# Kernel optimization log

Measured on AMD Instinct MI355X. Metric: run time of the kernel, lower is better.

## Reference

```python
import jax, jax.numpy as jnp
import numpy as np

SOS = 1
H = 1024   # hidden_size
V = 32000  # vocab_size
B = 64     # batch
S = 50     # encoder (source) length
T = 25     # decode steps (target length)


def setup_inputs() -> dict:
    key = jax.random.key(0)
    ks = jax.random.split(key, 16)
    s = 1.0 / np.sqrt(H)

    def u(k, shape):
        return jax.random.uniform(k, shape, jnp.float32, -s, s)

    return {
        "encoder_outputs": jax.random.normal(ks[0], (B, S, H), jnp.float32),
        "encoder_hidden": jax.random.normal(ks[1], (1, B, H), jnp.float32),
        "target_tensor": jax.random.randint(ks[2], (B, T), 0, V),
        "emb": jax.random.normal(ks[3], (V, H), jnp.float32),       # nn.Embedding
        "Wa": u(ks[4], (H, H)), "ba": u(ks[5], (H,)),               # attention query proj
        "Ua": u(ks[6], (H, H)), "bu": u(ks[7], (H,)),               # attention key proj
        "Va": u(ks[8], (H, 1)), "bv": u(ks[9], (1,)),               # attention score vector
        "W_ih": u(ks[10], (3 * H, 2 * H)), "b_ih": u(ks[11], (3 * H,)),  # GRU input weights
        "W_hh": u(ks[12], (3 * H, H)), "b_hh": u(ks[13], (3 * H,)),     # GRU hidden weights
        "Wout": u(ks[14], (V, H)), "bout": u(ks[15], (V,)),         # output linear
    }


def reference(encoder_outputs, encoder_hidden, target_tensor, emb,
              Wa, ba, Ua, bu, Va, bv, W_ih, b_ih, W_hh, b_hh, Wout, bout):
    # Bahdanau key projection is independent of the decode step: precompute once.
    keys_proj = encoder_outputs @ Ua.T + bu        # [B, S, H]
    h0 = encoder_hidden[0]                         # [B, H]

    # Teacher forcing: input at step i is SOS then target[:, :-1]. (Dropout in eval mode = identity.)
    sos = jnp.full((B, 1), SOS, dtype=target_tensor.dtype)
    tokens = jnp.concatenate([sos, target_tensor[:, :-1]], axis=1).T  # [T, B]

    def step(h, tok):
        x_emb = emb[tok]                                         # [B, H]
        q = h @ Wa.T + ba                                        # [B, H] (query = hidden)
        scores = jnp.tanh(q[:, None, :] + keys_proj) @ Va        # [B, S, 1]
        w = jax.nn.softmax(scores[..., 0] + bv[0], axis=-1)      # [B, S]
        context = jnp.einsum('bs,bsh->bh', w, encoder_outputs)   # [B, H]
        x = jnp.concatenate([x_emb, context], axis=-1)           # [B, 2H]
        gx = x @ W_ih.T + b_ih                                   # [B, 3H]
        gh = h @ W_hh.T + b_hh                                   # [B, 3H]
        rx, zx, nx = jnp.split(gx, 3, axis=-1)                   # PyTorch gate order r,z,n
        rh, zh, nh = jnp.split(gh, 3, axis=-1)
        r = jax.nn.sigmoid(rx + rh)
        z = jax.nn.sigmoid(zx + zh)
        n = jnp.tanh(nx + r * nh)
        h_new = (1.0 - z) * n + z * h
        logits = h_new @ Wout.T + bout                           # [B, V]
        return h_new, logits

    _, logits = jax.lax.scan(step, h0, tokens)                   # [T, B, V]
    return jnp.transpose(logits, (1, 0, 2))                      # [B, T, V]
```

## Files before the change

kernel.cpp:

```cpp
#include <hip/hip_runtime.h>
#include <hip/hip_bf16.h>

#define BB_ 64
#define SS_ 50
#define TT_ 25
#define HH_ 1024
#define VV_ 32000

typedef __bf16 bf16x8 __attribute__((ext_vector_type(8)));
typedef float f32x4 __attribute__((ext_vector_type(4)));
typedef unsigned long long u64;

__device__ __forceinline__ unsigned short f2b(float f) {
  unsigned u = __float_as_uint(f);
  u = (u + 0x7FFFu + ((u >> 16) & 1u)) >> 16;
  return (unsigned short)u;
}
__device__ __forceinline__ float b2f_(unsigned short s) {
  return __uint_as_float((unsigned)s << 16);
}
__device__ __forceinline__ float fast_tanh(float x) {
  float e = __expf(2.f * x);
  return 1.f - 2.f / (e + 1.f);
}
__device__ __forceinline__ float fast_sigmoid(float x) {
  return 1.f / (1.f + __expf(-x));
}
__device__ __forceinline__ void gload16(const void* g, void* l) {
  __builtin_amdgcn_global_load_lds((const __attribute__((address_space(1))) void*)g,
                                   (__attribute__((address_space(3))) void*)l, 16, 0, 0);
}
__device__ __forceinline__ bf16x8 ldb8(const unsigned short* p) {
  return *(const bf16x8*)p;
}

__device__ __forceinline__ void cstf(float* p, float v) {
  __hip_atomic_store(p, v, __ATOMIC_RELAXED, __HIP_MEMORY_SCOPE_AGENT);
}
__device__ __forceinline__ void cst4(unsigned* p, unsigned v) {
  __hip_atomic_store(p, v, __ATOMIC_RELAXED, __HIP_MEMORY_SCOPE_AGENT);
}
__device__ __forceinline__ unsigned cadd(unsigned* p) {
  return __hip_atomic_fetch_add(p, 1u, __ATOMIC_RELAXED, __HIP_MEMORY_SCOPE_AGENT);
}
__device__ __forceinline__ unsigned cldu(const unsigned* p) {
  return __hip_atomic_load(p, __ATOMIC_RELAXED, __HIP_MEMORY_SCOPE_AGENT);
}

#define CNT_ROOT 256
#define CNT_EPOCH 288
#define CNT_QBAR 320
#define CNT_MINI 384

__device__ __forceinline__ void gbarG(unsigned* cnt, unsigned n) {
  __syncthreads();
  if (threadIdx.x == 0) {
    unsigned g = blockIdx.x & 7u;
    unsigned old = cadd(cnt + g * 32);
    if (old == n * 32u - 1u) {
      unsigned r = cadd(cnt + CNT_ROOT);
      if (r == n * 8u - 1u) cst4(cnt + CNT_EPOCH, n);
    }
    while (cldu(cnt + CNT_EPOCH) < n) __builtin_amdgcn_s_sleep(2);
  }
  __syncthreads();
}

__global__ __launch_bounds__(256) void cvt_bf16(const float* __restrict__ src,
                                                unsigned short* __restrict__ dst, long n) {
  long i = ((long)blockIdx.x * 256 + threadIdx.x) * 4;
  if (i >= n) return;
  float4 v = *(const float4*)(src + i);
  *(ushort4*)(dst + i) = make_ushort4(f2b(v.x), f2b(v.y), f2b(v.z), f2b(v.w));
}

__global__ __launch_bounds__(256) void embed_gather(const int* __restrict__ tgt,
                                                    const float* __restrict__ emb,
                                                    unsigned short* __restrict__ X) {
  long idx = ((long)blockIdx.x * 256 + threadIdx.x) * 4;
  if (idx >= (long)1600 * HH_) return;
  int col = (int)(idx & (HH_ - 1));
  int r = (int)(idx >> 10);
  int t = r % 25;
  int tok = (t == 0) ? 1 : tgt[r - 1];
  float4 v = *(const float4*)(emb + (long)tok * HH_ + col);
  *(ushort4*)(X + idx) = make_ushort4(f2b(v.x), f2b(v.y), f2b(v.z), f2b(v.w));
}

__global__ __launch_bounds__(256) void init_h(const float* __restrict__ eh,
                                              unsigned short* __restrict__ HBROT,
                                              unsigned* __restrict__ cnt) {
  if (blockIdx.x == 0) {
    for (int k = threadIdx.x; k < 4096; k += 256) cnt[k] = 0;
  }
  int i = (blockIdx.x * 256 + threadIdx.x) * 4;
  if (i >= BB_ * HH_) return;
  float4 v = *(const float4*)(eh + i);
  *(ushort4*)(HBROT + i) = make_ushort4(f2b(v.x), f2b(v.y), f2b(v.z), f2b(v.w));
}

__global__ __launch_bounds__(256) void gemm128_bt(
    const unsigned short* __restrict__ A, const unsigned short* __restrict__ W,
    const float* __restrict__ bias, float* __restrict__ out, long ldo,
    int Mtiles, int ldw, int Mvalid) {
  __shared__ __align__(16) unsigned short As[128 * 32];
  __shared__ __align__(16) unsigned short Bs[128 * 32];
  int nwg = gridDim.x;
  int orig = blockIdx.x;
  int xcd = orig & 7, lid = orig >> 3;
  int qq = nwg >> 3, rr = nwg & 7;
  int wgid = (xcd < rr ? xcd * (qq + 1) : rr * (qq + 1) + (xcd - rr) * qq) + lid;
  int m0 = (wgid % Mtiles) * 128;
  int n0 = (wgid / Mtiles) * 128;
  int tid = threadIdx.x;
  int w = tid >> 6, l = tid & 63;
  int srow = tid >> 2, scg = tid & 3;
  int mw = (w & 1) * 64, nw = (w >> 1) * 64;

  const unsigned short* Ag0 = A + (long)(m0 + srow) * 1024 + scg * 8;
  const unsigned short* Ag1 = Ag0 + 64 * 1024;
  const unsigned short* Wg0 = W + (long)(n0 + srow) * ldw + scg * 8;
  const unsigned short* Wg1 = Wg0 + (long)64 * ldw;
  unsigned short* lA0 = As + tid * 8;
  unsigned short* lA1 = As + 2048 + tid * 8;
  unsigned short* lB0 = Bs + tid * 8;
  unsigned short* lB1 = Bs + 2048 + tid * 8;

  f32x4 zero = {0.f, 0.f, 0.f, 0.f};
  f32x4 acc[4][4];
#pragma unroll
  for (int i = 0; i < 4; ++i)
#pragma unroll
    for (int j = 0; j < 4; ++j) acc[i][j] = zero;

  for (int k0 = 0; k0 < 1024; k0 += 32) {
    __syncthreads();
    gload16(Ag0 + k0, lA0);
    gload16(Ag1 + k0, lA1);
    gload16(Wg0 + k0, lB0);
    gload16(Wg1 + k0, lB1);
    __syncthreads();
    bf16x8 af[4], bg[4];
#pragma unroll
    for (int mt = 0; mt < 4; ++mt)
      af[mt] = ldb8(As + (mw + mt * 16 + (l & 15)) * 32 + (l >> 4) * 8);
#pragma unroll
    for (int nt = 0; nt < 4; ++nt)
      bg[nt] = ldb8(Bs + (nw + nt * 16 + (l & 15)) * 32 + (l >> 4) * 8);
#pragma unroll
    for (int mt = 0; mt < 4; ++mt)
#pragma unroll
      for (int nt = 0; nt < 4; ++nt)
        acc[mt][nt] = __builtin_amdgcn_mfma_f32_16x16x32_bf16(af[mt], bg[nt], acc[mt][nt], 0, 0, 0);
  }

  int lr = (l >> 4) * 4, lc = l & 15;
#pragma unroll
  for (int nt = 0; nt < 4; ++nt) {
    int col = n0 + nw + nt * 16 + lc;
    float bv = bias[col];
#pragma unroll
    for (int mt = 0; mt < 4; ++mt) {
#pragma unroll
      for (int r = 0; r < 4; ++r) {
        int m = m0 + mw + mt * 16 + lr + r;
        if (m < Mvalid) out[(long)m * ldo + col] = acc[mt][nt][r] + bv;
      }
    }
  }
}

__global__ __launch_bounds__(256) void decode_loop(
    const unsigned short* __restrict__ WaB, const unsigned short* __restrict__ WhhB,
    const unsigned short* __restrict__ WihB, const float* __restrict__ ba,
    const float* __restrict__ bhh, const float* __restrict__ Va,
    const unsigned short* __restrict__ KEYSB, const unsigned short* __restrict__ ENCB,
    const float* __restrict__ GA, const float* __restrict__ ehid,
    float* __restrict__ QROT, float* __restrict__ GHROT, float* __restrict__ SCROT,
    unsigned short* __restrict__ CTXROT, unsigned short* __restrict__ HBROT,
    unsigned short* __restrict__ HALLB, unsigned* __restrict__ cnt) {
  __shared__ __align__(16) char AsC[16 * 2048];
  __shared__ float qs[1024];
  __shared__ float vas[1024];
  __shared__ float wgt[64];

  const int tid = threadIdx.x, bid = blockIdx.x;
  const int wv = tid >> 6, l = tid & 63;
  const int lc = l & 15, hi = l >> 4, ko = hi * 8, lr4 = hi * 4;
  const int xcd = bid & 7, lxb = bid >> 3;
  const int mt_ = lxb & 3, cg = lxb >> 2;

  const int m1 = mt_ * 16;
  const int nch = xcd * 32 + cg * 4 + wv;
  const int n1 = nch * 16;
  const bool isq = (n1 < 1024);
  const unsigned short* B1 = isq ? WaB + (long)(n1 + lc) * 1024 + ko
                                 : WhhB + (long)(n1 - 1024 + lc) * 1024 + ko;
  float* o1 = isq ? QROT + n1 : GHROT + (n1 - 1024);
  const long ldo1 = isq ? 1024 : 3072;
  const long slot1 = isq ? (long)BB_ * 1024 : (long)BB_ * 3072;
  const float bv1 = isq ? ba[n1 + lc] : bhh[n1 - 1024 + lc];

  const int b2 = xcd * 8 + cg;
  const int jq = mt_ * 4 + wv;
  const int c2 = mt_ * 256 + tid;

  const int m3 = mt_ * 16, n3 = (xcd * 8 + cg) * 16;
  const unsigned short* Bg0 = WihB + (long)(n3 + lc) * 2048 + 1024 + ko;
  const unsigned short* Bg1 = Bg0 + (long)1024 * 2048;
  const unsigned short* Bg2 = Bg0 + (long)2048 * 2048;
  const int ig = n3 + lc;
  float hreg[4];
  if (tid < 64) {
#pragma unroll
    for (int r = 0; r < 4; ++r) hreg[r] = ehid[(long)(m3 + lr4 + r) * HH_ + ig];
  }

#pragma unroll
  for (int j = 0; j < 4; ++j) vas[tid + j * 256] = Va[tid + j * 256];

  const f32x4 zero = {0.f, 0.f, 0.f, 0.f};
  unsigned gB = 0;

  for (int t = 0; t < TT_; ++t) {
    {
      const unsigned short* hbase = HBROT + (long)t * (BB_ * 1024);
#pragma unroll
      for (int i = 0; i < 16; ++i) {
        u64 v = *((const u64*)(hbase + (long)(m1 + i) * 1024) + tid);
        *(u64*)(AsC + ((i * 2048 + tid * 8) ^ ((i & 7) << 4))) = v;
      }
      __syncthreads();
      f32x4 acc = zero;
#pragma unroll 8
      for (int k = 0; k < 1024; k += 32) {
        bf16x8 af = *(const bf16x8*)(AsC + ((lc * 2048 + (k + ko) * 2) ^ ((lc & 7) << 4)));
        acc = __builtin_amdgcn_mfma_f32_16x16x32_bf16(af, ldb8(B1 + k), acc, 0, 0, 0);
      }
#pragma unroll
      for (int r = 0; r < 4; ++r)
        cstf(o1 + (long)t * slot1 + (long)(m1 + lr4 + r) * ldo1 + lc, acc[r] + bv1);
    }
    __syncthreads();
    if (tid == 0) {
      if (xcd < 2) cadd(cnt + CNT_QBAR);
      while (cldu(cnt + CNT_QBAR) < (unsigned)(t + 1) * 64u) __builtin_amdgcn_s_sleep(2);
    }
    __syncthreads();

    {
      const float* qsl = QROT + (long)t * (BB_ * 1024) + (long)b2 * 1024;
#pragma unroll
      for (int j = 0; j < 4; ++j)
        qs[tid + j * 256] = qsl[tid + j * 256];
      __syncthreads();
      for (int s = jq; s < SS_; s += 16) {
        const unsigned short* kr = KEYSB + ((long)b2 * SS_ + s) * 1024;
        float p = 0.f;
#pragma unroll
        for (int j = 0; j < 16; ++j) {
          int hh = l + j * 64;
          p += fast_tanh(qs[hh] + b2f_(kr[hh])) * vas[hh];
        }
#pragma unroll
        for (int off = 32; off; off >>= 1) p += __shfl_down(p, off);
        if (l == 0) cstf(SCROT + (long)t * 4096 + b2 * 64 + s, p);
      }
    }
    __syncthreads();
    if (tid == 0) {
      unsigned* mc = cnt + CNT_MINI + b2 * 32;
      cadd(mc);
      while (cldu(mc) < (unsigned)(t + 1) * 4u) __builtin_amdgcn_s_sleep(2);
    }
    __syncthreads();

    {
      if (tid < 64) {
        float v = (tid < SS_) ? SCROT[(long)t * 4096 + b2 * 64 + tid] : -1e30f;
        float m = v;
#pragma unroll
        for (int off = 32; off; off >>= 1) m = fmaxf(m, __shfl_down(m, off));
        m = __shfl(m, 0);
        float e = (tid < SS_) ? __expf(v - m) : 0.f;
        float ssum = e;
#pragma unroll
        for (int off = 32; off; off >>= 1) ssum += __shfl_down(ssum, off);
        ssum = __shfl(ssum, 0);
        if (tid < SS_) wgt[tid] = e / ssum;
      }
      __syncthreads();
      {
        const unsigned short* ep = ENCB + (long)b2 * SS_ * 1024 + c2;
        float a0 = 0.f;
#pragma unroll 10
        for (int s = 0; s < SS_; ++s)
          a0 += wgt[s] * b2f_(ep[(long)s * 1024]);
        unsigned hb16 = (unsigned)f2b(a0);
        unsigned ob = (unsigned)__shfl_xor((int)hb16, 1);
        if ((tid & 1) == 0)
          cst4((unsigned*)(CTXROT + (long)t * (BB_ * 1024) + (long)b2 * 1024 + c2), hb16 | (ob << 16));
      }
    }
    gbarG(cnt, ++gB);

    {
      const unsigned short* cbase = CTXROT + (long)t * (BB_ * 1024);
#pragma unroll
      for (int i = 0; i < 16; ++i) {
        u64 v = *((const u64*)(cbase + (long)(m3 + i) * 1024) + tid);
        *(u64*)(AsC + ((i * 2048 + tid * 8) ^ ((i & 7) << 4))) = v;
      }
      __syncthreads();
      if (tid < 64) {
        f32x4 ar = zero, az = zero, an_ = zero;
#pragma unroll 8
        for (int k = 0; k < 1024; k += 32) {
          bf16x8 a = *(const bf16x8*)(AsC + ((lc * 2048 + (k + ko) * 2) ^ ((lc & 7) << 4)));
          ar = __builtin_amdgcn_mfma_f32_16x16x32_bf16(a, ldb8(Bg0 + k), ar, 0, 0, 0);
          az = __builtin_amdgcn_mfma_f32_16x16x32_bf16(a, ldb8(Bg1 + k), az, 0, 0, 0);
          an_ = __builtin_amdgcn_mfma_f32_16x16x32_bf16(a, ldb8(Bg2 + k), an_, 0, 0, 0);
        }
        const float* ghb = GHROT + (long)t * (BB_ * 3072);
        unsigned short* hnb = HBROT + (long)(t + 1) * (BB_ * 1024);
#pragma unroll
        for (int r = 0; r < 4; ++r) {
          int bb = m3 + lr4 + r;
          long rowBT = (long)bb * TT_ + t;
          const float* ga = GA + rowBT * 3072;
          const float* gh = ghb + (long)bb * 3072;
          float rr = fast_sigmoid(ga[ig] + ar[r] + gh[ig]);
          float zz = fast_sigmoid(ga[1024 + ig] + az[r] + gh[1024 + ig]);
          float nn = fast_tanh(ga[2048 + ig] + an_[r] + rr * gh[2048 + ig]);
          float hnew = (1.f - zz) * nn + zz * hreg[r];
          hreg[r] = hnew;
          unsigned hb = (unsigned)f2b(hnew);
          unsigned ob = (unsigned)__shfl_xor((int)hb, 1);
          if ((lc & 1) == 0)
            cst4((unsigned*)(hnb + (long)bb * 1024 + ig), hb | (ob << 16));
          HALLB[rowBT * HH_ + ig] = (unsigned short)hb;
        }
      }
    }
    if (t < TT_ - 1) gbarG(cnt, ++gB);
  }
}

extern "C" void kernel_launch(void* const* d_in, const int* in_sizes, int n_in,
                              void* d_out, int out_size, void* d_ws, size_t ws_size,
                              hipStream_t stream) {
  (void)in_sizes; (void)n_in; (void)out_size; (void)ws_size;
  const float* enc  = (const float*)d_in[0];
  const float* ehid = (const float*)d_in[1];
  const int*   tgt  = (const int*)d_in[2];
  const float* emb  = (const float*)d_in[3];
  const float* Wa   = (const float*)d_in[4];
  const float* ba   = (const float*)d_in[5];
  const float* Ua   = (const float*)d_in[6];
  const float* bu   = (const float*)d_in[7];
  const float* Va   = (const float*)d_in[8];
  const float* Wih  = (const float*)d_in[10];
  const float* bih  = (const float*)d_in[11];
  const float* Whh  = (const float*)d_in[12];
  const float* bhh  = (const float*)d_in[13];
  const float* Wout = (const float*)d_in[14];
  const float* bout = (const float*)d_in[15];
  float* out = (float*)d_out;

  char* p = (char*)d_ws;
  auto alloc = [&](size_t bytes) { char* r = p; p += (bytes + 255) & ~(size_t)255; return r; };
  unsigned short* WOUTB = (unsigned short*)alloc((size_t)VV_ * HH_ * 2);
  unsigned short* WIHB  = (unsigned short*)alloc((size_t)3072 * 2048 * 2);
  unsigned short* WHHB  = (unsigned short*)alloc((size_t)3072 * 1024 * 2);
  unsigned short* WAB   = (unsigned short*)alloc((size_t)1024 * 1024 * 2);
  unsigned short* UAB   = (unsigned short*)alloc((size_t)1024 * 1024 * 2);
  unsigned short* ENCB  = (unsigned short*)alloc((size_t)BB_ * SS_ * HH_ * 2);
  unsigned short* XEMB  = (unsigned short*)alloc((size_t)1664 * HH_ * 2);
  unsigned short* HALLB = (unsigned short*)alloc((size_t)1664 * HH_ * 2);
  float* KEYS = (float*)alloc((size_t)BB_ * SS_ * HH_ * 4);
  unsigned short* KEYSB = (unsigned short*)alloc((size_t)BB_ * SS_ * HH_ * 2);
  float* GA   = (float*)alloc((size_t)1600 * 3072 * 4);
  float* QROT  = (float*)alloc((size_t)TT_ * BB_ * 1024 * 4);
  float* GHROT = (float*)alloc((size_t)TT_ * BB_ * 3072 * 4);
  float* SCROT = (float*)alloc((size_t)TT_ * 4096 * 4);
  unsigned short* CTXROT = (unsigned short*)alloc((size_t)TT_ * BB_ * 1024 * 2);
  unsigned short* HBROT  = (unsigned short*)alloc((size_t)(TT_ + 1) * BB_ * 1024 * 2);
  unsigned* CNT = (unsigned*)alloc(4096 * 4);

  auto cvt = [&](const float* s, unsigned short* d, long n) {
    cvt_bf16<<<dim3((unsigned)((n / 4 + 255) / 256)), dim3(256), 0, stream>>>(s, d, n);
  };
  cvt(Wout, WOUTB, (long)VV_ * HH_);
  cvt(Wih, WIHB, (long)3072 * 2048);
  cvt(Whh, WHHB, (long)3072 * 1024);
  cvt(Wa, WAB, (long)1024 * 1024);
  cvt(Ua, UAB, (long)1024 * 1024);
  cvt(enc, ENCB, (long)BB_ * SS_ * HH_);
  embed_gather<<<dim3(1600 * HH_ / 4 / 256), dim3(256), 0, stream>>>(tgt, emb, XEMB);
  init_h<<<dim3(BB_ * HH_ / 4 / 256), dim3(256), 0, stream>>>(ehid, HBROT, CNT);

  gemm128_bt<<<dim3(25 * 8), dim3(256), 0, stream>>>(ENCB, UAB, bu, KEYS, (long)1024, 25, 1024, 3200);
  cvt(KEYS, KEYSB, (long)BB_ * SS_ * HH_);
  gemm128_bt<<<dim3(13 * 24), dim3(256), 0, stream>>>(XEMB, WIHB, bih, GA, (long)3072, 13, 2048, 1600);

  decode_loop<<<dim3(256), dim3(256), 0, stream>>>(
      WAB, WHHB, WIHB, ba, bhh, Va, KEYSB, ENCB, GA, ehid,
      QROT, GHROT, SCROT, CTXROT, HBROT, HALLB, CNT);

  gemm128_bt<<<dim3(13 * 250), dim3(256), 0, stream>>>(HALLB, WOUTB, bout, out, (long)VV_, 13, 1024, 1600);
}
```

Baseline: 1.657 ms.

## Replace global grid barriers with per-row-tile dependency flag counters

```diff
diff --git a/kernel.cpp b/kernel.cpp
--- a/kernel.cpp
+++ b/kernel.cpp
@@ -47,24 +47,11 @@
   return __hip_atomic_load(p, __ATOMIC_RELAXED, __HIP_MEMORY_SCOPE_AGENT);
 }
 
-#define CNT_ROOT 256
-#define CNT_EPOCH 288
-#define CNT_QBAR 320
-#define CNT_MINI 384
-
-__device__ __forceinline__ void gbarG(unsigned* cnt, unsigned n) {
-  __syncthreads();
-  if (threadIdx.x == 0) {
-    unsigned g = blockIdx.x & 7u;
-    unsigned old = cadd(cnt + g * 32);
-    if (old == n * 32u - 1u) {
-      unsigned r = cadd(cnt + CNT_ROOT);
-      if (r == n * 8u - 1u) cst4(cnt + CNT_EPOCH, n);
-    }
-    while (cldu(cnt + CNT_EPOCH) < n) __builtin_amdgcn_s_sleep(2);
-  }
-  __syncthreads();
-}
+#define F_QR   0
+#define F_GHR  128
+#define F_CTXR 256
+#define F_HR   384
+#define F_MINI 512
 
 __global__ __launch_bounds__(256) void cvt_bf16(const float* __restrict__ src,
                                                 unsigned short* __restrict__ dst, long n) {
@@ -189,6 +176,7 @@
   const int lc = l & 15, hi = l >> 4, ko = hi * 8, lr4 = hi * 4;
   const int xcd = bid & 7, lxb = bid >> 3;
   const int mt_ = lxb & 3, cg = lxb >> 2;
+  const int qcls = xcd >> 1;
 
   const int m1 = mt_ * 16;
   const int nch = xcd * 32 + cg * 4 + wv;
@@ -220,9 +208,13 @@
   for (int j = 0; j < 4; ++j) vas[tid + j * 256] = Va[tid + j * 256];
 
   const f32x4 zero = {0.f, 0.f, 0.f, 0.f};
-  unsigned gB = 0;
 
   for (int t = 0; t < TT_; ++t) {
+    if (tid == 0) {
+      while (cldu(cnt + F_HR + mt_ * 32) < (unsigned)t * 64u) __builtin_amdgcn_s_sleep(4);
+    }
+    __syncthreads();
+
     {
       const unsigned short* hbase = HBROT + (long)t * (BB_ * 1024);
 #pragma unroll
@@ -243,8 +235,8 @@
     }
     __syncthreads();
     if (tid == 0) {
-      if (xcd < 2) cadd(cnt + CNT_QBAR);
-      while (cldu(cnt + CNT_QBAR) < (unsigned)(t + 1) * 64u) __builtin_amdgcn_s_sleep(2);
+      cadd(cnt + (isq ? F_QR : F_GHR) + mt_ * 32);
+      while (cldu(cnt + F_QR + qcls * 32) < (unsigned)(t + 1) * 16u) __builtin_amdgcn_s_sleep(4);
     }
     __syncthreads();
 
@@ -269,9 +261,9 @@
     }
     __syncthreads();
     if (tid == 0) {
-      unsigned* mc = cnt + CNT_MINI + b2 * 32;
+      unsigned* mc = cnt + F_MINI + b2 * 32;
       cadd(mc);
-      while (cldu(mc) < (unsigned)(t + 1) * 4u) __builtin_amdgcn_s_sleep(2);
+      while (cldu(mc) < (unsigned)(t + 1) * 4u) __builtin_amdgcn_s_sleep(4);
     }
     __syncthreads();
 
@@ -302,7 +294,13 @@
           cst4((unsigned*)(CTXROT + (long)t * (BB_ * 1024) + (long)b2 * 1024 + c2), hb16 | (ob << 16));
       }
     }
-    gbarG(cnt, ++gB);
+    __syncthreads();
+    if (tid == 0) {
+      cadd(cnt + F_CTXR + qcls * 32);
+      while (cldu(cnt + F_CTXR + mt_ * 32) < (unsigned)(t + 1) * 64u) __builtin_amdgcn_s_sleep(4);
+      while (cldu(cnt + F_GHR + mt_ * 32) < (unsigned)(t + 1) * 48u) __builtin_amdgcn_s_sleep(4);
+    }
+    __syncthreads();
 
     {
       const unsigned short* cbase = CTXROT + (long)t * (BB_ * 1024);
@@ -342,7 +340,8 @@
         }
       }
     }
-    if (t < TT_ - 1) gbarG(cnt, ++gB);
+    __syncthreads();
+    if (tid == 0) cadd(cnt + F_HR + mt_ * 32);
   }
 }
 
```

New measurement: 1.660 ms. About the same (+0.2%).
